# Optimization experiments

Hardware: AMD Instinct MI355X
Metric: run time of the kernel (lower is better)

## Reference

```python
import jax, jax.numpy as jnp
import numpy as np

LOCAL_SIZE = 120


def setup_inputs() -> dict:
    key = jax.random.key(0)
    k1, k2, k3 = jax.random.split(key, 3)
    B, C, H, W = 32, 32, 480, 480
    local_map = jax.random.normal(k1, (B, C, H, W), dtype=jnp.float32)
    # Channel 1 is the agent-position map: a small blob of exact 1.0s per sample.
    # Clear channel 1 then stamp 3x3 blocks of ones at random centers (some near
    # borders so the shrink+interpolate path is exercised).
    local_map = local_map.at[:, 1].set(0.0)
    ys = jax.random.randint(k2, (B,), 2, H - 2)
    xs = jax.random.randint(k3, (B,), 2, W - 2)
    # force a few samples near the boundary
    ys = ys.at[0].set(5).at[1].set(H - 5)
    xs = xs.at[0].set(5).at[2].set(W - 5)
    dy, dx = jnp.meshgrid(jnp.arange(-1, 2), jnp.arange(-1, 2), indexing='ij')
    bi = jnp.repeat(jnp.arange(B), 9)
    yi = (ys[:, None, None] + dy[None]).reshape(-1)
    xi = (xs[:, None, None] + dx[None]).reshape(-1)
    local_map = local_map.at[bi, 1, yi, xi].set(1.0)
    return {"local_map": local_map}


def _agent_pos(local_map):
    # centroid (rounded) of pixels == 1 in channel 1; fallback to center
    B, C, H, W = local_map.shape
    cur = local_map[:, 1]
    mask = (cur == 1.0).astype(jnp.float32)  # [B,H,W]
    cnt = mask.sum(axis=(1, 2))
    ygrid = jnp.arange(H, dtype=jnp.float32)[None, :, None]
    xgrid = jnp.arange(W, dtype=jnp.float32)[None, None, :]
    denom = jnp.maximum(cnt, 1.0)
    my = jnp.round((mask * ygrid).sum(axis=(1, 2)) / denom)
    mx = jnp.round((mask * xgrid).sum(axis=(1, 2)) / denom)
    py = jnp.where(cnt > 0, my, H // 2).astype(jnp.int32)
    px = jnp.where(cnt > 0, mx, W // 2).astype(jnp.int32)
    return py, px


def _crop_resize(img, y_start, ry, x_start, rx):
    # img: [C,H,W]; bilinear-resample the region [y_start:y_start+ry, x_start:x_start+rx]
    # to (L,L) with align_corners=False semantics (identity when ry==rx==L).
    L = LOCAL_SIZE
    i = jnp.arange(L, dtype=jnp.float32) + 0.5
    sy = jnp.maximum(i * (ry.astype(jnp.float32) / L) - 0.5, 0.0)
    sx = jnp.maximum(i * (rx.astype(jnp.float32) / L) - 0.5, 0.0)
    y0 = jnp.floor(sy).astype(jnp.int32)
    x0 = jnp.floor(sx).astype(jnp.int32)
    y1 = jnp.minimum(y0 + 1, ry - 1)
    x1 = jnp.minimum(x0 + 1, rx - 1)
    wy = (sy - y0.astype(jnp.float32))[:, None]   # [L,1]
    wx = (sx - x0.astype(jnp.float32))[None, :]   # [1,L]
    ya0, ya1 = y_start + y0, y_start + y1
    xa0, xa1 = x_start + x0, x_start + x1
    v00 = img[:, ya0[:, None], xa0[None, :]]
    v01 = img[:, ya0[:, None], xa1[None, :]]
    v10 = img[:, ya1[:, None], xa0[None, :]]
    v11 = img[:, ya1[:, None], xa1[None, :]]
    top = v00 * (1.0 - wx) + v01 * wx
    bot = v10 * (1.0 - wx) + v11 * wx
    return top * (1.0 - wy) + bot * wy  # [C,L,L]


def reference(local_map) -> jnp.ndarray:
    B, C, H, W = local_map.shape
    half = LOCAL_SIZE // 2
    py, px = _agent_pos(local_map)
    y_start = jnp.maximum(py - half, 0)
    y_end = jnp.minimum(py + half, H)
    x_start = jnp.maximum(px - half, 0)
    x_end = jnp.minimum(px + half, W)
    ry = y_end - y_start
    rx = x_end - x_start
    return jax.vmap(_crop_resize)(local_map, y_start, ry, x_start, rx)
```

## Files before the change

kernel.cpp:

```cpp
#include <hip/hip_runtime.h>

#define Hh 480
#define Ww 480
#define Cc 32
#define Bb 32
#define Ll 120
#define CHUNKS 15

__global__ __launch_bounds__(256) void agent_pos_partial(const float* __restrict__ in,
                                                         int* __restrict__ part) {
    const int b     = blockIdx.x / CHUNKS;
    const int chunk = blockIdx.x % CHUNKS;
    const float4* ch = (const float4*)(in + ((size_t)b * Cc + 1) * (size_t)(Hh * Ww));
    const int base = chunk * (Hh * Ww / CHUNKS / 4);

    int cnt = 0, sy = 0, sx = 0;
#pragma unroll
    for (int it = 0; it < 15; ++it) {
        const int fidx = base + it * 256 + threadIdx.x;
        const float4 v = ch[fidx];
        const int lin = fidx * 4;
        if (v.x == 1.0f) { cnt++; sy += (lin    ) / Ww; sx += (lin    ) % Ww; }
        if (v.y == 1.0f) { cnt++; sy += (lin + 1) / Ww; sx += (lin + 1) % Ww; }
        if (v.z == 1.0f) { cnt++; sy += (lin + 2) / Ww; sx += (lin + 2) % Ww; }
        if (v.w == 1.0f) { cnt++; sy += (lin + 3) / Ww; sx += (lin + 3) % Ww; }
    }
#pragma unroll
    for (int off = 32; off > 0; off >>= 1) {
        cnt += __shfl_down(cnt, off);
        sy  += __shfl_down(sy,  off);
        sx  += __shfl_down(sx,  off);
    }
    __shared__ int lds[4][3];
    const int wave = threadIdx.x >> 6;
    const int lane = threadIdx.x & 63;
    if (lane == 0) { lds[wave][0] = cnt; lds[wave][1] = sy; lds[wave][2] = sx; }
    __syncthreads();
    if (threadIdx.x == 0) {
        int c = 0, y = 0, x = 0;
#pragma unroll
        for (int w = 0; w < 4; ++w) { c += lds[w][0]; y += lds[w][1]; x += lds[w][2]; }
        int* o = part + ((size_t)b * CHUNKS + chunk) * 3;
        o[0] = c; o[1] = y; o[2] = x;
    }
}

__global__ __launch_bounds__(128) void crop_resize(const float* __restrict__ in,
                                                   const int* __restrict__ part,
                                                   float* __restrict__ out) {
    const int b  = blockIdx.x / Ll;
    const int yo = blockIdx.x % Ll;

    int cnt = 0, sy = 0, sx = 0;
    const int* p = part + (size_t)b * CHUNKS * 3;
#pragma unroll
    for (int i = 0; i < CHUNKS; ++i) { cnt += p[i*3]; sy += p[i*3+1]; sx += p[i*3+2]; }

    const float denom = fmaxf((float)cnt, 1.0f);
    const int py = (cnt > 0) ? (int)rintf((float)sy / denom) : (Hh / 2);
    const int px = (cnt > 0) ? (int)rintf((float)sx / denom) : (Ww / 2);

    const int y_start = max(py - Ll / 2, 0);
    const int y_end   = min(py + Ll / 2, Hh);
    const int x_start = max(px - Ll / 2, 0);
    const int x_end   = min(px + Ll / 2, Ww);
    const int ry = y_end - y_start;
    const int rx = x_end - x_start;

    const float iy  = (float)yo + 0.5f;
    const float syf = fmaxf(iy * ((float)ry / (float)Ll) - 0.5f, 0.0f);
    const int   y0  = (int)floorf(syf);
    const int   y1  = min(y0 + 1, ry - 1);
    const float wy  = syf - (float)y0;
    const int   ya0 = y_start + y0;
    const int   ya1 = y_start + y1;

    const int x = threadIdx.x;
    if (x >= Ll) return;

    const float ix  = (float)x + 0.5f;
    const float sxf = fmaxf(ix * ((float)rx / (float)Ll) - 0.5f, 0.0f);
    const int   x0  = (int)floorf(sxf);
    const int   x1  = min(x0 + 1, rx - 1);
    const float wx  = sxf - (float)x0;
    const int   xa0 = x_start + x0;
    const int   xa1 = x_start + x1;

    const float* img = in + (size_t)b * Cc * Hh * Ww;
    float* ob = out + (size_t)b * Cc * Ll * Ll + (size_t)yo * Ll + x;

    const int r0 = ya0 * Ww;
    const int r1 = ya1 * Ww;
#pragma unroll 4
    for (int c = 0; c < Cc; ++c) {
        const float* pc = img + (size_t)c * Hh * Ww;
        const float v00 = pc[r0 + xa0];
        const float v01 = pc[r0 + xa1];
        const float v10 = pc[r1 + xa0];
        const float v11 = pc[r1 + xa1];
        const float top = v00 * (1.0f - wx) + v01 * wx;
        const float bot = v10 * (1.0f - wx) + v11 * wx;
        ob[(size_t)c * Ll * Ll] = top * (1.0f - wy) + bot * wy;
    }
}

extern "C" void kernel_launch(void* const* d_in, const int* in_sizes, int n_in,
                              void* d_out, int out_size, void* d_ws, size_t ws_size,
                              hipStream_t stream) {
    const float* in  = (const float*)d_in[0];
    float*       out = (float*)d_out;
    int*         part = (int*)d_ws;

    agent_pos_partial<<<Bb * CHUNKS, 256, 0, stream>>>(in, part);
    crop_resize<<<Bb * Ll, 128, 0, stream>>>(in, part, out);
}
```

Before: 1.029 ms.

## Stage crop region per (batch, channel) in LDS before bilinear resampling

The crop-resize kernel now uses one 512-thread block per (batch, channel) pair instead of one block per output row. Each block copies the up-to-120x120 crop window into a padded shared-memory tile with coalesced row loads, then resamples from LDS. This avoids the four scattered global gathers per output pixel and the redundant reads of neighbouring rows. In exchange each block needs about 58 KB of LDS, which limits occupancy, and it adds a barrier between the load and compute phases.

```diff
diff --git a/kernel.cpp b/kernel.cpp
--- a/kernel.cpp
+++ b/kernel.cpp
@@ -6,6 +6,7 @@
 #define Bb 32
 #define Ll 120
 #define CHUNKS 15
+#define PITCH 121
 
 __global__ __launch_bounds__(256) void agent_pos_partial(const float* __restrict__ in,
                                                          int* __restrict__ part) {
@@ -45,11 +46,11 @@
     }
 }
 
-__global__ __launch_bounds__(128) void crop_resize(const float* __restrict__ in,
-                                                   const int* __restrict__ part,
-                                                   float* __restrict__ out) {
-    const int b  = blockIdx.x / Ll;
-    const int yo = blockIdx.x % Ll;
+__global__ __launch_bounds__(512) void crop_resize_lds(const float* __restrict__ in,
+                                                       const int* __restrict__ part,
+                                                       float* __restrict__ out) {
+    const int bc = blockIdx.x;
+    const int b  = bc >> 5;
 
     int cnt = 0, sy = 0, sx = 0;
     const int* p = part + (size_t)b * CHUNKS * 3;
@@ -67,40 +68,52 @@
     const int ry = y_end - y_start;
     const int rx = x_end - x_start;
 
-    const float iy  = (float)yo + 0.5f;
-    const float syf = fmaxf(iy * ((float)ry / (float)Ll) - 0.5f, 0.0f);
-    const int   y0  = (int)floorf(syf);
-    const int   y1  = min(y0 + 1, ry - 1);
-    const float wy  = syf - (float)y0;
-    const int   ya0 = y_start + y0;
-    const int   ya1 = y_start + y1;
+    __shared__ float tile[Ll * PITCH];
 
-    const int x = threadIdx.x;
-    if (x >= Ll) return;
+    const int t = threadIdx.x;
+    const float* src = in + (size_t)bc * (Hh * Ww) + (size_t)y_start * Ww + x_start;
 
-    const float ix  = (float)x + 0.5f;
-    const float sxf = fmaxf(ix * ((float)rx / (float)Ll) - 0.5f, 0.0f);
-    const int   x0  = (int)floorf(sxf);
-    const int   x1  = min(x0 + 1, rx - 1);
-    const float wx  = sxf - (float)x0;
-    const int   xa0 = x_start + x0;
-    const int   xa1 = x_start + x1;
+    {
+        const int r0   = t >> 7;
+        const int xcol = t & 127;
+        if (xcol < rx) {
+            for (int r = r0; r < ry; r += 4) {
+                tile[r * PITCH + xcol] = src[(size_t)r * Ww + xcol];
+            }
+        }
+    }
+    __syncthreads();
 
-    const float* img = in + (size_t)b * Cc * Hh * Ww;
-    float* ob = out + (size_t)b * Cc * Ll * Ll + (size_t)yo * Ll + x;
+    if (t < 4 * Ll) {
+        const int tyo = t / Ll;
+        const int xo  = t - tyo * Ll;
 
-    const int r0 = ya0 * Ww;
-    const int r1 = ya1 * Ww;
-#pragma unroll 4
-    for (int c = 0; c < Cc; ++c) {
-        const float* pc = img + (size_t)c * Hh * Ww;
-        const float v00 = pc[r0 + xa0];
-        const float v01 = pc[r0 + xa1];
-        const float v10 = pc[r1 + xa0];
-        const float v11 = pc[r1 + xa1];
-        const float top = v00 * (1.0f - wx) + v01 * wx;
-        const float bot = v10 * (1.0f - wx) + v11 * wx;
-        ob[(size_t)c * Ll * Ll] = top * (1.0f - wy) + bot * wy;
+        const float ix  = (float)xo + 0.5f;
+        const float sxf = fmaxf(ix * ((float)rx / (float)Ll) - 0.5f, 0.0f);
+        const int   x0  = (int)floorf(sxf);
+        const int   x1  = min(x0 + 1, rx - 1);
+        const float wx  = sxf - (float)x0;
+
+        const float ry_scale = (float)ry / (float)Ll;
+        float* ob = out + (size_t)bc * (Ll * Ll) + xo;
+
+        for (int yo = tyo; yo < Ll; yo += 4) {
+            const float iy  = (float)yo + 0.5f;
+            const float syf = fmaxf(iy * ry_scale - 0.5f, 0.0f);
+            const int   y0  = (int)floorf(syf);
+            const int   y1  = min(y0 + 1, ry - 1);
+            const float wy  = syf - (float)y0;
+
+            const float* row0 = tile + y0 * PITCH;
+            const float* row1 = tile + y1 * PITCH;
+            const float v00 = row0[x0];
+            const float v01 = row0[x1];
+            const float v10 = row1[x0];
+            const float v11 = row1[x1];
+            const float top = v00 * (1.0f - wx) + v01 * wx;
+            const float bot = v10 * (1.0f - wx) + v11 * wx;
+            ob[(size_t)yo * Ll] = top * (1.0f - wy) + bot * wy;
+        }
     }
 }
 
@@ -112,5 +125,5 @@
     int*         part = (int*)d_ws;
 
     agent_pos_partial<<<Bb * CHUNKS, 256, 0, stream>>>(in, part);
-    crop_resize<<<Bb * Ll, 128, 0, stream>>>(in, part, out);
+    crop_resize_lds<<<Bb * Cc, 512, 0, stream>>>(in, part, out);
 }
```

Result: no change. 1.029 ms (-0.1%).
